# Performance work log

Hardware: AMD Instinct MI355X
Metric: run time of the kernel (lower is better)

The kernel has to match this reference:

```python
import jax, jax.numpy as jnp
import numpy as np

N = 100000   # nodes
E = 1600000  # edges
DIN = 128    # input features
H = 64       # hidden dim
C = 10       # classes
G = 512      # graphs in batch


def setup_inputs() -> dict:
    key = jax.random.key(0)
    ks = jax.random.split(key, 9)
    x = jax.random.normal(ks[0], (N, DIN), jnp.float32)
    edge_index = jax.random.randint(ks[1], (2, E), 0, N, dtype=jnp.int64)
    batch = jnp.sort(jax.random.randint(ks[2], (N,), 0, G, dtype=jnp.int64))
    W1 = jax.random.normal(ks[3], (DIN, H), jnp.float32) / np.sqrt(DIN).astype(np.float32)
    b1 = jnp.zeros((H,), jnp.float32)
    W2 = jax.random.normal(ks[4], (H, H), jnp.float32) / np.sqrt(H).astype(np.float32)
    b2 = jnp.zeros((H,), jnp.float32)
    Wl = jax.random.normal(ks[5], (H, C), jnp.float32) / np.sqrt(H).astype(np.float32)
    bl = jnp.zeros((C,), jnp.float32)
    return {"x": x, "edge_index": edge_index, "batch": batch,
            "W1": W1, "b1": b1, "W2": W2, "b2": b2, "Wl": Wl, "bl": bl}


def _gcn_conv(x, W, b, src, dst, norm):
    # transform then symmetric-normalized gather/scatter-add (PyG GCNConv)
    h = x @ W                          # [N, H]
    msg = h[src] * norm[:, None]       # [E+N, H] gather
    return jax.ops.segment_sum(msg, dst, num_segments=N) + b


def reference(x, edge_index, batch, W1, b1, W2, b2, Wl, bl):
    loop = jnp.arange(N, dtype=edge_index.dtype)
    src = jnp.concatenate([edge_index[0], loop])  # add self-loops
    dst = jnp.concatenate([edge_index[1], loop])
    deg = jax.ops.segment_sum(jnp.ones_like(dst, dtype=x.dtype), dst, num_segments=N)
    dinv = jnp.where(deg > 0, jax.lax.rsqrt(deg), 0.0)
    norm = dinv[src] * dinv[dst]                  # D^-1/2 (A+I) D^-1/2 weights

    h = jax.nn.relu(_gcn_conv(x, W1, b1, src, dst, norm))
    # dropout is identity in eval mode
    h = jax.nn.relu(_gcn_conv(h, W2, b2, src, dst, norm))

    counts = jax.ops.segment_sum(jnp.ones((N,), x.dtype), batch, num_segments=G)
    pooled = jax.ops.segment_sum(h, batch, num_segments=G) / jnp.maximum(counts, 1.0)[:, None]
    return pooled @ Wl + bl  # [G, C]
```

## Files before the change

kernel.cpp:

```cpp
#include <hip/hip_runtime.h>
#include <hip/hip_bf16.h>
#include <cstdint>

#define DIN 128
#define HD 64
#define NCLS 10
#define BSH 9
#define BIN_CHUNK 4096


__global__ __launch_bounds__(256)
void bucket_count_k(const int* __restrict__ dst, int* __restrict__ bktcnt,
                    int E, int nbkt) {
  __shared__ int h[256];
  const int t = threadIdx.x;
  h[t] = 0;
  __syncthreads();
  const int base = blockIdx.x * BIN_CHUNK;
  #pragma unroll
  for (int j = 0; j < 16; ++j) {
    int idx = base + j * 256 + t;
    if (idx < E) atomicAdd(&h[dst[idx] >> BSH], 1);
  }
  __syncthreads();
  if (t < nbkt && h[t]) atomicAdd(&bktcnt[t], h[t]);
}

__global__ __launch_bounds__(256)
void bucket_scan_k(const int* __restrict__ bktcnt, int* __restrict__ bktoff,
                   int* __restrict__ gcursor, int* __restrict__ rowstart,
                   int nbkt, int n, int E) {
  __shared__ int s[256];
  const int t = threadIdx.x;
  int v = (t < nbkt) ? bktcnt[t] : 0;
  s[t] = v;
  __syncthreads();
  for (int o = 1; o < 256; o <<= 1) {
    int u = (t >= o) ? s[t - o] : 0;
    __syncthreads();
    s[t] += u;
    __syncthreads();
  }
  int ex = s[t] - v;
  if (t < nbkt) { bktoff[t] = ex; gcursor[t] = ex; }
  if (t == 0)   { bktoff[nbkt] = E; rowstart[n] = E; }
}

__global__ __launch_bounds__(256)
void bin_k(const int* __restrict__ src, const int* __restrict__ dst,
           int* __restrict__ gcursor, unsigned int* __restrict__ binned,
           int E, int nbkt) {
  __shared__ int cnt[256], off[256], gb[256], s[256];
  __shared__ unsigned int pk_lds[BIN_CHUNK];
  __shared__ unsigned char sb[BIN_CHUNK];
  const int t = threadIdx.x;
  const int base = blockIdx.x * BIN_CHUNK;
  const int m = min(BIN_CHUNK, E - base);
  cnt[t] = 0;
  __syncthreads();
  unsigned int pk[16]; int bb[16]; int rk[16];
  #pragma unroll
  for (int j = 0; j < 16; ++j) {
    int idx = base + j * 256 + t;
    if (idx < E) {
      int d = dst[idx];
      int sv = src[idx];
      bb[j] = d >> BSH;
      pk[j] = ((unsigned)sv << BSH) | (unsigned)(d & ((1 << BSH) - 1));
      rk[j] = atomicAdd(&cnt[bb[j]], 1);
    } else bb[j] = -1;
  }
  __syncthreads();
  s[t] = cnt[t];
  __syncthreads();
  for (int o = 1; o < 256; o <<= 1) {
    int v = (t >= o) ? s[t - o] : 0;
    __syncthreads();
    s[t] += v;
    __syncthreads();
  }
  off[t] = s[t] - cnt[t];
  if (t < nbkt && cnt[t] > 0) gb[t] = atomicAdd(&gcursor[t], cnt[t]);
  __syncthreads();
  #pragma unroll
  for (int j = 0; j < 16; ++j) {
    if (bb[j] >= 0) {
      int p = off[bb[j]] + rk[j];
      pk_lds[p] = pk[j];
      sb[p] = (unsigned char)bb[j];
    }
  }
  __syncthreads();
  for (int i = t; i < m; i += 256) {
    int b = sb[i];
    binned[gb[b] + (i - off[b])] = pk_lds[i];
  }
}

__global__ __launch_bounds__(256)
void bucket_csr_k(const unsigned int* __restrict__ binned,
                  const int* __restrict__ bktoff,
                  int* __restrict__ rowstart, float* __restrict__ dinv,
                  int* __restrict__ csr_src, int n) {
  __shared__ int lcnt[512], loff[512], lcur[512], s[256];
  const int t = threadIdx.x;
  const int b = blockIdx.x;
  const int node0 = b << BSH;
  const int s0 = bktoff[b];
  const int e0 = bktoff[b + 1];
  const int cnt = e0 - s0;
  lcnt[t] = 0; lcnt[t + 256] = 0;
  lcur[t] = 0; lcur[t + 256] = 0;
  __syncthreads();
  for (int i = t; i < cnt; i += 256)
    atomicAdd(&lcnt[binned[s0 + i] & ((1 << BSH) - 1)], 1);
  __syncthreads();
  int a0 = lcnt[2 * t], a1 = lcnt[2 * t + 1];
  s[t] = a0 + a1;
  __syncthreads();
  for (int o = 1; o < 256; o <<= 1) {
    int v = (t >= o) ? s[t - o] : 0;
    __syncthreads();
    s[t] += v;
    __syncthreads();
  }
  int ex = s[t] - (a0 + a1);
  loff[2 * t] = ex;
  loff[2 * t + 1] = ex + a0;
  __syncthreads();
  #pragma unroll
  for (int i = t; i < 512; i += 256) {
    int node = node0 + i;
    if (node < n) {
      rowstart[node] = s0 + loff[i];
      dinv[node] = rsqrtf((float)(lcnt[i] + 1));
    }
  }
  for (int i = t; i < cnt; i += 256) {
    unsigned int pk = binned[s0 + i];
    int ld = pk & ((1 << BSH) - 1);
    int r = atomicAdd(&lcur[ld], 1);
    csr_src[s0 + loff[ld] + r] = (int)(pk >> BSH);
  }
}


template<int K>
__global__ __launch_bounds__(256)
void gemm_rowscale_k(const float* __restrict__ X, const float* __restrict__ W,
                     const float* __restrict__ dinv, __hip_bfloat16* __restrict__ out16,
                     int n) {
  __shared__ float sW[K * HD];
  __shared__ float sX[64 * 65];
  const int t  = threadIdx.x;
  const int tx = t & 15;
  const int ty = t >> 4;
  const int row0 = blockIdx.x * 64;

  for (int idx = t; idx < K * HD / 4; idx += 256)
    reinterpret_cast<float4*>(sW)[idx] = reinterpret_cast<const float4*>(W)[idx];

  float acc[4][4] = {};
  for (int kt = 0; kt < K; kt += 64) {
    __syncthreads();
    #pragma unroll
    for (int m = 0; m < 4; ++m) {
      int el = (m * 256 + t) * 4;
      int r = el >> 6, c = el & 63;
      float4 v;
      if (row0 + r < n) v = *reinterpret_cast<const float4*>(&X[(size_t)(row0 + r) * K + kt + c]);
      else              v = make_float4(0.f, 0.f, 0.f, 0.f);
      float* p = &sX[r * 65 + c];
      p[0] = v.x; p[1] = v.y; p[2] = v.z; p[3] = v.w;
    }
    __syncthreads();
    for (int k = 0; k < 64; ++k) {
      float4 w4 = *reinterpret_cast<const float4*>(&sW[(kt + k) * HD + tx * 4]);
      #pragma unroll
      for (int rr = 0; rr < 4; ++rr) {
        float a = sX[(ty * 4 + rr) * 65 + k];
        acc[rr][0] = fmaf(a, w4.x, acc[rr][0]);
        acc[rr][1] = fmaf(a, w4.y, acc[rr][1]);
        acc[rr][2] = fmaf(a, w4.z, acc[rr][2]);
        acc[rr][3] = fmaf(a, w4.w, acc[rr][3]);
      }
    }
  }
  #pragma unroll
  for (int rr = 0; rr < 4; ++rr) {
    int r = row0 + ty * 4 + rr;
    if (r < n) {
      float s = dinv[r];
      __hip_bfloat16 o[4];
      o[0] = __float2bfloat16(acc[rr][0] * s);
      o[1] = __float2bfloat16(acc[rr][1] * s);
      o[2] = __float2bfloat16(acc[rr][2] * s);
      o[3] = __float2bfloat16(acc[rr][3] * s);
      *reinterpret_cast<ushort4*>(&out16[(size_t)r * HD + tx * 4]) =
          *reinterpret_cast<ushort4*>(o);
    }
  }
}


__global__ __launch_bounds__(256)
void aggregate_k(const __hip_bfloat16* __restrict__ g, const int* __restrict__ rowstart,
                 const int* __restrict__ csr_src, const float* __restrict__ dinv,
                 const float* __restrict__ bias, float* __restrict__ out, int n) {
  const int lane = threadIdx.x & 63;
  const int d = (blockIdx.x * 256 + threadIdx.x) >> 6;
  if (d >= n) return;
  const int p0 = rowstart[d], p1 = rowstart[d + 1];
  float acc = __bfloat162float(g[(size_t)d * HD + lane]);
  int p = p0;
  for (; p + 8 <= p1; p += 8) {
    int s0 = csr_src[p],     s1 = csr_src[p + 1], s2 = csr_src[p + 2], s3 = csr_src[p + 3];
    int s4 = csr_src[p + 4], s5 = csr_src[p + 5], s6 = csr_src[p + 6], s7 = csr_src[p + 7];
    float a0 = __bfloat162float(g[(size_t)s0 * HD + lane]);
    float a1 = __bfloat162float(g[(size_t)s1 * HD + lane]);
    float a2 = __bfloat162float(g[(size_t)s2 * HD + lane]);
    float a3 = __bfloat162float(g[(size_t)s3 * HD + lane]);
    float a4 = __bfloat162float(g[(size_t)s4 * HD + lane]);
    float a5 = __bfloat162float(g[(size_t)s5 * HD + lane]);
    float a6 = __bfloat162float(g[(size_t)s6 * HD + lane]);
    float a7 = __bfloat162float(g[(size_t)s7 * HD + lane]);
    acc += ((a0 + a1) + (a2 + a3)) + ((a4 + a5) + (a6 + a7));
  }
  for (; p < p1; ++p) acc += __bfloat162float(g[(size_t)csr_src[p] * HD + lane]);
  out[(size_t)d * HD + lane] = fmaxf(fmaf(dinv[d], acc, bias[lane]), 0.f);
}


__global__ __launch_bounds__(256)
void poolhead_k(const float* __restrict__ h, const int* __restrict__ batch,
                const float* __restrict__ Wl, const float* __restrict__ bl,
                float* __restrict__ outp, int n) {
  const int gi = blockIdx.x;
  const int lane = threadIdx.x & 63;
  const int w = threadIdx.x >> 6;
  int lo = 0, hi = n;
  while (lo < hi) { int mid = (lo + hi) >> 1; if (batch[mid] < gi) lo = mid + 1; else hi = mid; }
  const int start = lo;
  hi = n;
  while (lo < hi) { int mid = (lo + hi) >> 1; if (batch[mid] < gi + 1) lo = mid + 1; else hi = mid; }
  const int end = lo;
  float acc = 0.f;
  for (int i = start + w; i < end; i += 4) acc += h[(size_t)i * HD + lane];
  __shared__ float red[4][HD];
  __shared__ float pooled[HD];
  red[w][lane] = acc;
  __syncthreads();
  if (w == 0) {
    float s = red[0][lane] + red[1][lane] + red[2][lane] + red[3][lane];
    pooled[lane] = s / fmaxf((float)(end - start), 1.f);
  }
  __syncthreads();
  const int t = threadIdx.x;
  if (t < NCLS) {
    float s = bl[t];
    #pragma unroll
    for (int j = 0; j < HD; ++j) s = fmaf(pooled[j], Wl[j * NCLS + t], s);
    outp[gi * NCLS + t] = s;
  }
}


extern "C" void kernel_launch(void* const* d_in, const int* in_sizes, int n_in,
                              void* d_out, int out_size, void* d_ws, size_t ws_size,
                              hipStream_t stream) {
  const float* x   = (const float*)d_in[0];
  const int*   ei  = (const int*)d_in[1];
  const int* batch = (const int*)d_in[2];
  const float* W1  = (const float*)d_in[3];
  const float* b1  = (const float*)d_in[4];
  const float* W2  = (const float*)d_in[5];
  const float* b2  = (const float*)d_in[6];
  const float* Wl  = (const float*)d_in[7];
  const float* bl  = (const float*)d_in[8];
  const int N = in_sizes[0] / DIN;
  const int E = in_sizes[1] / 2;
  const int G = out_size / NCLS;
  const int* src = ei;
  const int* dst = ei + E;
  const int nbkt = (N + (1 << BSH) - 1) >> BSH;

  char* ws = (char*)d_ws;
  size_t off = 0;
  auto alloc = [&](size_t bytes) -> char* {
    char* p = ws + off;
    off += (bytes + 255) & ~size_t(255);
    return p;
  };
  int*   rowstart = (int*)alloc(sizeof(int) * (N + 1));
  int*   csr_src  = (int*)alloc(sizeof(int) * E);
  float* dinv     = (float*)alloc(sizeof(float) * N);
  __hip_bfloat16* A16 = (__hip_bfloat16*)alloc(sizeof(__hip_bfloat16) * (size_t)N * HD);
  float* B        = (float*)alloc(sizeof(float) * (size_t)N * HD);
  int*   bktcnt   = (int*)alloc(sizeof(int) * nbkt);
  int*   bktoff   = (int*)alloc(sizeof(int) * (nbkt + 1));
  int*   gcursor  = (int*)alloc(sizeof(int) * nbkt);
  unsigned int* binned = (unsigned int*)A16;

  const int nchunks = (E + BIN_CHUNK - 1) / BIN_CHUNK;
  hipMemsetAsync(bktcnt, 0, sizeof(int) * nbkt, stream);
  bucket_count_k<<<nchunks, 256, 0, stream>>>(dst, bktcnt, E, nbkt);
  bucket_scan_k<<<1, 256, 0, stream>>>(bktcnt, bktoff, gcursor, rowstart, nbkt, N, E);
  bin_k<<<nchunks, 256, 0, stream>>>(src, dst, gcursor, binned, E, nbkt);
  bucket_csr_k<<<nbkt, 256, 0, stream>>>(binned, bktoff, rowstart, dinv, csr_src, N);

  gemm_rowscale_k<DIN><<<(N + 63) / 64, 256, 0, stream>>>(x, W1, dinv, A16, N);
  aggregate_k<<<(N + 3) / 4, 256, 0, stream>>>(A16, rowstart, csr_src, dinv, b1, B, N);

  gemm_rowscale_k<HD><<<(N + 63) / 64, 256, 0, stream>>>(B, W2, dinv, A16, N);
  aggregate_k<<<(N + 3) / 4, 256, 0, stream>>>(A16, rowstart, csr_src, dinv, b2, B, N);

  poolhead_k<<<G, 256, 0, stream>>>(B, batch, Wl, bl, (float*)d_out, N);
}
```

Baseline: 359.7 us.

## Aggregate two nodes per wave with packed bf16x2 loads and shuffled indices

The aggregation kernel now splits each 64-lane wave into two 32-lane halves, each handling one destination node and loading two bf16 features per lane as a 32-bit word. Neighbor indices are fetched cooperatively, 32 at a time, with one coalesced load per half-wave and broadcast via shuffles, replacing per-lane scalar index loads. This halves the wave count, widens memory accesses, and cuts redundant index traffic. The cost is divergence between halves with different degrees and a fully unrolled, predicated 32-step inner loop.

```diff
diff --git a/kernel.cpp b/kernel.cpp
--- a/kernel.cpp
+++ b/kernel.cpp
@@ -208,26 +208,34 @@
                  const int* __restrict__ csr_src, const float* __restrict__ dinv,
                  const float* __restrict__ bias, float* __restrict__ out, int n) {
   const int lane = threadIdx.x & 63;
-  const int d = (blockIdx.x * 256 + threadIdx.x) >> 6;
+  const int hl   = lane & 31;
+  const int wave = (blockIdx.x * 256 + threadIdx.x) >> 6;
+  const int d    = wave * 2 + (lane >> 5);
   if (d >= n) return;
   const int p0 = rowstart[d], p1 = rowstart[d + 1];
-  float acc = __bfloat162float(g[(size_t)d * HD + lane]);
-  int p = p0;
-  for (; p + 8 <= p1; p += 8) {
-    int s0 = csr_src[p],     s1 = csr_src[p + 1], s2 = csr_src[p + 2], s3 = csr_src[p + 3];
-    int s4 = csr_src[p + 4], s5 = csr_src[p + 5], s6 = csr_src[p + 6], s7 = csr_src[p + 7];
-    float a0 = __bfloat162float(g[(size_t)s0 * HD + lane]);
-    float a1 = __bfloat162float(g[(size_t)s1 * HD + lane]);
-    float a2 = __bfloat162float(g[(size_t)s2 * HD + lane]);
-    float a3 = __bfloat162float(g[(size_t)s3 * HD + lane]);
-    float a4 = __bfloat162float(g[(size_t)s4 * HD + lane]);
-    float a5 = __bfloat162float(g[(size_t)s5 * HD + lane]);
-    float a6 = __bfloat162float(g[(size_t)s6 * HD + lane]);
-    float a7 = __bfloat162float(g[(size_t)s7 * HD + lane]);
-    acc += ((a0 + a1) + (a2 + a3)) + ((a4 + a5) + (a6 + a7));
-  }
-  for (; p < p1; ++p) acc += __bfloat162float(g[(size_t)csr_src[p] * HD + lane]);
-  out[(size_t)d * HD + lane] = fmaxf(fmaf(dinv[d], acc, bias[lane]), 0.f);
+
+  unsigned int v = *reinterpret_cast<const unsigned int*>(&g[(size_t)d * HD + hl * 2]);
+  float ax = __uint_as_float(v << 16);
+  float ay = __uint_as_float(v & 0xffff0000u);
+
+  for (int p = p0; p < p1; p += 32) {
+    const int nrem = p1 - p;
+    int idx = (hl < nrem) ? csr_src[p + hl] : 0;
+    #pragma unroll
+    for (int j = 0; j < 32; ++j) {
+      if (j < nrem) {
+        int s = __shfl(idx, j, 32);
+        unsigned int w = *reinterpret_cast<const unsigned int*>(&g[(size_t)s * HD + hl * 2]);
+        ax += __uint_as_float(w << 16);
+        ay += __uint_as_float(w & 0xffff0000u);
+      }
+    }
+  }
+  const float dv = dinv[d];
+  float2 o;
+  o.x = fmaxf(fmaf(dv, ax, bias[hl * 2]), 0.f);
+  o.y = fmaxf(fmaf(dv, ay, bias[hl * 2 + 1]), 0.f);
+  *reinterpret_cast<float2*>(&out[(size_t)d * HD + hl * 2]) = o;
 }
 
 
@@ -309,10 +317,10 @@
   bucket_csr_k<<<nbkt, 256, 0, stream>>>(binned, bktoff, rowstart, dinv, csr_src, N);
 
   gemm_rowscale_k<DIN><<<(N + 63) / 64, 256, 0, stream>>>(x, W1, dinv, A16, N);
-  aggregate_k<<<(N + 3) / 4, 256, 0, stream>>>(A16, rowstart, csr_src, dinv, b1, B, N);
+  aggregate_k<<<(N + 7) / 8, 256, 0, stream>>>(A16, rowstart, csr_src, dinv, b1, B, N);
 
   gemm_rowscale_k<HD><<<(N + 63) / 64, 256, 0, stream>>>(B, W2, dinv, A16, N);
-  aggregate_k<<<(N + 3) / 4, 256, 0, stream>>>(A16, rowstart, csr_src, dinv, b2, B, N);
+  aggregate_k<<<(N + 7) / 8, 256, 0, stream>>>(A16, rowstart, csr_src, dinv, b2, B, N);
 
   poolhead_k<<<G, 256, 0, stream>>>(B, batch, Wl, bl, (float*)d_out, N);
 }
```

Measured after the change: 349.2 us. 2.9% less time.
